# Kernel optimization log

Measured on AMD Instinct MI355X. Metric: run time of the kernel, lower is better.

## Reference

```python
import jax, jax.numpy as jnp
import numpy as np

N_EMBED = 1024
HEAD_SIZE = 64
SEQ_LEN = 4096
BATCH = 4


def setup_inputs() -> dict:
    key = jax.random.key(0)
    ks = jax.random.split(key, 7)
    scale = 1.0 / np.sqrt(N_EMBED)
    return {
        "x": jax.random.normal(ks[0], (BATCH, SEQ_LEN, N_EMBED), dtype=jnp.float32),
        "Wq": jax.random.normal(ks[1], (N_EMBED, HEAD_SIZE), dtype=jnp.float32) * scale,
        "bq": jax.random.normal(ks[2], (HEAD_SIZE,), dtype=jnp.float32) * 0.01,
        "Wk": jax.random.normal(ks[3], (N_EMBED, HEAD_SIZE), dtype=jnp.float32) * scale,
        "bk": jax.random.normal(ks[4], (HEAD_SIZE,), dtype=jnp.float32) * 0.01,
        "Wv": jax.random.normal(ks[5], (N_EMBED, HEAD_SIZE), dtype=jnp.float32) * scale,
        "bv": jax.random.normal(ks[6], (HEAD_SIZE,), dtype=jnp.float32) * 0.01,
    }


def reference(x, Wq, bq, Wk, bk, Wv, bv):
    # q, k, v: [B, S, H]
    q = x @ Wq + bq
    k = x @ Wk + bk
    v = x @ Wv + bv
    # raw scores [B, S, S]; original masks to -inf THEN divides by sqrt(head_size)
    # (-inf / sqrt = -inf, so equivalent to scaling finite entries only)
    scores = jnp.einsum("bqh,bkh->bqk", q, k)
    seq_len = x.shape[1]
    causal = jnp.tril(jnp.ones((seq_len, seq_len), dtype=bool))
    inv_scale = 1.0 / jnp.sqrt(jnp.asarray(HEAD_SIZE, dtype=scores.dtype))
    scores = jnp.where(causal, scores * inv_scale, -jnp.inf)
    weight = jax.nn.softmax(scores, axis=-1)
    # dropout is identity in eval / p=0
    out = jnp.einsum("bqk,bkh->bqh", weight, v)
    return out
```

## Files before the change

kernel.cpp:

```cpp
#include <hip/hip_runtime.h>
#include <hip/hip_bf16.h>

#define SS 4096
#define NROW 16384

typedef __attribute__((ext_vector_type(8))) short short8;
typedef __attribute__((ext_vector_type(4))) float f32x4;

#define AS1 __attribute__((address_space(1)))
#define AS3 __attribute__((address_space(3)))

static __device__ __forceinline__ void glds16(const void* g, void* l) {
    __builtin_amdgcn_global_load_lds((const AS1 unsigned*)g, (AS3 unsigned*)l, 16, 0, 0);
}
static __device__ __forceinline__ short f2bf(float f) {
    union { float f; unsigned u; } v; v.f = f;
    unsigned r = v.u + 0x7FFFu + ((v.u >> 16) & 1u);
    return (short)(r >> 16);
}
static __device__ __forceinline__ short f2bf_fast(float f) {
    union { float f; unsigned u; } v; v.f = f;
    return (short)((v.u + 0x8000u) >> 16);
}
static __device__ __forceinline__ unsigned pkbf(float lo, float hi) {
    union { float f; unsigned u; } x, y; x.f = lo; y.f = hi;
    return __builtin_amdgcn_perm(y.u + 0x8000u, x.u + 0x8000u, 0x07060302);
}
static __device__ __forceinline__ float bf2f(short s) {
    union { unsigned u; float f; } v;
    v.u = ((unsigned)(unsigned short)s) << 16;
    return v.f;
}

__global__ __launch_bounds__(256) void pack_w(const float* __restrict__ Wq,
                                              const float* __restrict__ Wk,
                                              const float* __restrict__ Wv,
                                              short* __restrict__ Wpack) {
    __shared__ float T[64 * 65];
    int bid = blockIdx.x;
    int nb = bid >> 4, kb = bid & 15;
    const float* W = (nb == 0) ? Wq : (nb == 1 ? Wk : Wv);
    int n0 = nb * 64, k0 = kb * 64;
    int tid = threadIdx.x;
    for (int ps = 0; ps < 16; ++ps) {
        int idx = tid + ps * 256;
        int kk = idx >> 6, nn = idx & 63;
        T[kk * 65 + nn] = W[(k0 + kk) * 64 + nn];
    }
    __syncthreads();
    for (int ps = 0; ps < 16; ++ps) {
        int idx = tid + ps * 256;
        int nn = idx >> 6, kk = idx & 63;
        Wpack[(n0 + nn) * 1024 + k0 + kk] = f2bf(T[kk * 65 + nn]);
    }
}

__global__ __launch_bounds__(256, 2) void proj_qkv(const float* __restrict__ x,
                                                   const short* __restrict__ Wpack,
                                                   const float* __restrict__ bq,
                                                   const float* __restrict__ bk,
                                                   const float* __restrict__ bv,
                                                   short* __restrict__ Qg,
                                                   short* __restrict__ Kg,
                                                   short* __restrict__ Vt) {
    __shared__ float Xs[2][32 * 64];
    __shared__ short Wsm[2][192 * 64];
    int tid = threadIdx.x, lane = tid & 63, wv = tid >> 6;
    int g = lane >> 4, c = lane & 15;
    int mh = wv & 1, nh = wv >> 1;
    int rowbase = blockIdx.x * 32;

    f32x4 acc[6];
    for (int i = 0; i < 6; ++i) acc[i] = (f32x4)(0.f);

    int xs0 = (wv * 2 + 0) * 64 + lane, xs1 = (wv * 2 + 1) * 64 + lane;
    int xr0 = xs0 >> 4, xp0 = (xs0 & 15) ^ (xr0 & 15);
    int xr1 = xs1 >> 4, xp1 = (xs1 & 15) ^ (xr1 & 15);

#define PROJ_ISSUE(nbs, k0)                                                              \
    do {                                                                                 \
        glds16(x + (rowbase + xr0) * 1024 + (k0) + xp0 * 4, &Xs[nbs][(wv * 2 + 0) * 256]); \
        glds16(x + (rowbase + xr1) * 1024 + (k0) + xp1 * 4, &Xs[nbs][(wv * 2 + 1) * 256]); \
        for (int j = 0; j < 6; ++j) {                                                    \
            int ws = (wv * 6 + j) * 64 + lane;                                           \
            int wr = ws >> 3, wp = (ws & 7) ^ (wr & 7);                                  \
            glds16(Wpack + wr * 1024 + (k0) + wp * 8, &Wsm[nbs][(wv * 6 + j) * 512]);    \
        }                                                                                \
    } while (0)

    PROJ_ISSUE(0, 0);

    for (int ko = 0; ko < 16; ++ko) {
        int bs = ko & 1;
        __syncthreads();
        if (ko < 15) PROJ_ISSUE(bs ^ 1, (ko + 1) * 64);
        for (int kc = 0; kc < 2; ++kc) {
            int h0 = kc * 8 + g * 2;
            float4 xa = *reinterpret_cast<const float4*>(&Xs[bs][(mh * 16 + c) * 64 + ((h0) ^ c) * 4]);
            float4 xb = *reinterpret_cast<const float4*>(&Xs[bs][(mh * 16 + c) * 64 + ((h0 + 1) ^ c) * 4]);
            short8 a;
            unsigned* aw = (unsigned*)&a;
            aw[0] = pkbf(xa.x, xa.y); aw[1] = pkbf(xa.z, xa.w);
            aw[2] = pkbf(xb.x, xb.y); aw[3] = pkbf(xb.z, xb.w);
            for (int nt = 0; nt < 6; ++nt) {
                int wrow = nh * 96 + nt * 16 + c;
                short8 b = *reinterpret_cast<const short8*>(&Wsm[bs][wrow * 64 + ((g + 4 * kc) ^ (c & 7)) * 8]);
                acc[nt] = __builtin_amdgcn_mfma_f32_16x16x32_bf16(a, b, acc[nt], 0, 0, 0);
            }
        }
    }
#undef PROJ_ISSUE

    const float SCQ = 0.125f * 1.4426950408889634f;
    for (int nt = 0; nt < 6; ++nt) {
        int col = nh * 96 + nt * 16 + c;
        for (int r = 0; r < 4; ++r) {
            int grow = rowbase + mh * 16 + g * 4 + r;
            float vv = acc[nt][r];
            if (col < 64) {
                Qg[grow * 64 + col] = f2bf((vv + bq[col]) * SCQ);
            } else if (col < 128) {
                Kg[grow * 64 + (col - 64)] = f2bf(vv + bk[col - 64]);
            } else {
                int f = col - 128;
                int batch = grow >> 12, s = grow & 4095;
                Vt[batch * 262144 + (s >> 6) * 4096 + f * 64 + (s & 63)] = f2bf(vv + bv[f]);
            }
        }
    }
}

__global__ __launch_bounds__(256, 3) void attn(const short* __restrict__ Qg,
                                               const short* __restrict__ Kg,
                                               const short* __restrict__ Vt,
                                               short* __restrict__ Opart,
                                               float* __restrict__ Ls) {
    __shared__ short Kbuf[2][64 * 64];
    __shared__ short Vbuf[2][64 * 64];
    __shared__ short Ps[4][16 * 68];
    int tid = threadIdx.x, lane = tid & 63, wv = tid >> 6;
    int g = lane >> 4, c = lane & 15;

    int bid = blockIdx.x;
    int batch = bid / 288;
    int j = bid - batch * 288;
    int gq = (int)((sqrtf((float)j + 1.0f) - 1.0f) * 0.5f);
    while (4 * (gq + 1) * (gq + 2) <= j) ++gq;
    while (4 * gq * (gq + 1) > j) --gq;
    int rem = j - 4 * gq * (gq + 1);
    int pidx = rem / (gq + 1);
    int ch = rem - pidx * (gq + 1);
    int p = gq * 8 + pidx;

    int ntall = p + 1;
    int t0 = ch * 8, t1 = min(t0 + 8, ntall);
    int qrow0 = batch * SS + p * 64;
    const short* Kb = Kg + batch * SS * 64;
    const short* Vb = Vt + batch * SS * 64;

    short8 aq0 = *reinterpret_cast<const short8*>(Qg + (qrow0 + wv * 16 + c) * 64 + g * 8);
    short8 aq1 = *reinterpret_cast<const short8*>(Qg + (qrow0 + wv * 16 + c) * 64 + 32 + g * 8);

    f32x4 acc_o[4];
    for (int f = 0; f < 4; ++f) acc_o[f] = (f32x4)(0.f);
    float rs[4] = {0.f, 0.f, 0.f, 0.f};

    int s0 = (wv * 2 + 0) * 64 + lane, s1 = (wv * 2 + 1) * 64 + lane;
    int r0 = s0 >> 3, q0 = ((s0 & 7) ^ (r0 & 7));
    int r1 = s1 >> 3, q1 = ((s1 & 7) ^ (r1 & 7));

#define ATTN_ISSUE(nbs, t)                                                           \
    do {                                                                             \
        const short* kt_ = Kb + (t) * 4096;                                          \
        const short* vt_ = Vb + (t) * 4096;                                          \
        glds16(kt_ + r0 * 64 + q0 * 8, &Kbuf[nbs][(wv * 2 + 0) * 512]);              \
        glds16(kt_ + r1 * 64 + q1 * 8, &Kbuf[nbs][(wv * 2 + 1) * 512]);              \
        glds16(vt_ + r0 * 64 + q0 * 8, &Vbuf[nbs][(wv * 2 + 0) * 512]);              \
        glds16(vt_ + r1 * 64 + q1 * 8, &Vbuf[nbs][(wv * 2 + 1) * 512]);              \
    } while (0)

    ATTN_ISSUE(0, t0);
    short* Psw = Ps[wv];

    for (int t = t0; t < t1; ++t) {
        int bs = (t - t0) & 1;
        __syncthreads();
        if (t + 1 < t1) ATTN_ISSUE(bs ^ 1, t + 1);

        f32x4 s[4];
        for (int nt = 0; nt < 4; ++nt) s[nt] = (f32x4)(0.f);
        for (int nt = 0; nt < 4; ++nt) {
            short8 b0 = *reinterpret_cast<const short8*>(&Kbuf[bs][(nt * 16 + c) * 64 + ((g) ^ (c & 7)) * 8]);
            s[nt] = __builtin_amdgcn_mfma_f32_16x16x32_bf16(aq0, b0, s[nt], 0, 0, 0);
            short8 b1 = *reinterpret_cast<const short8*>(&Kbuf[bs][(nt * 16 + c) * 64 + ((g + 4) ^ (c & 7)) * 8]);
            s[nt] = __builtin_amdgcn_mfma_f32_16x16x32_bf16(aq1, b1, s[nt], 0, 0, 0);
        }

        if (t == p) {
            for (int nt = 0; nt < 4; ++nt)
                for (int r = 0; r < 4; ++r) {
                    int key = nt * 16 + c;
                    int row = wv * 16 + g * 4 + r;
                    float pv = (key <= row) ? __builtin_amdgcn_exp2f(s[nt][r]) : 0.f;
                    rs[r] += pv;
                    Psw[(g * 4 + r) * 68 + nt * 16 + c] = f2bf_fast(pv);
                }
        } else {
            for (int nt = 0; nt < 4; ++nt)
                for (int r = 0; r < 4; ++r) {
                    float pv = __builtin_amdgcn_exp2f(s[nt][r]);
                    rs[r] += pv;
                    Psw[(g * 4 + r) * 68 + nt * 16 + c] = f2bf_fast(pv);
                }
        }

        for (int kc2 = 0; kc2 < 2; ++kc2) {
            short8 ap = *reinterpret_cast<const short8*>(&Psw[c * 68 + kc2 * 32 + g * 8]);
            for (int f = 0; f < 4; ++f) {
                short8 bv_ = *reinterpret_cast<const short8*>(&Vbuf[bs][(f * 16 + c) * 64 + ((g + 4 * kc2) ^ (c & 7)) * 8]);
                acc_o[f] = __builtin_amdgcn_mfma_f32_16x16x32_bf16(ap, bv_, acc_o[f], 0, 0, 0);
            }
        }
    }
#undef ATTN_ISSUE

    float l[4];
    for (int r = 0; r < 4; ++r) {
        float ss = rs[r];
        ss += __shfl_xor(ss, 1);
        ss += __shfl_xor(ss, 2);
        ss += __shfl_xor(ss, 4);
        ss += __shfl_xor(ss, 8);
        l[r] = ss;
    }

    int slot = ((batch * 64 + p) << 3) + ch;
    short* op = Opart + slot * 4096;
    for (int r = 0; r < 4; ++r) {
        float inv = 1.0f / l[r];
        int row = wv * 16 + g * 4 + r;
        for (int f = 0; f < 4; ++f)
            op[row * 64 + f * 16 + c] = f2bf(acc_o[f][r] * inv);
    }
    if (c == 0)
        for (int r = 0; r < 4; ++r)
            Ls[slot * 64 + wv * 16 + g * 4 + r] = l[r];
}

__global__ __launch_bounds__(256) void merge_k(const short* __restrict__ Opart,
                                               const float* __restrict__ Ls,
                                               float* __restrict__ out) {
    int bP = blockIdx.x;
    int P = bP & 63, batch = bP >> 6;
    int nch = (P + 8) >> 3;
    int tid = threadIdx.x;
    int row = tid & 63, fg = tid >> 6;
    int slot0 = bP << 3;

    float w[8];
    float wsum = 0.f;
    for (int i = 0; i < nch; ++i) { w[i] = Ls[(slot0 + i) * 64 + row]; wsum += w[i]; }
    float invw = 1.0f / wsum;

    float o[16];
    for (int jj = 0; jj < 16; ++jj) o[jj] = 0.f;
    for (int i = 0; i < nch; ++i) {
        const short* op = Opart + (slot0 + i) * 4096 + row * 64 + fg * 16;
        short8 v0 = *reinterpret_cast<const short8*>(op);
        short8 v1 = *reinterpret_cast<const short8*>(op + 8);
        for (int jj = 0; jj < 8; ++jj) {
            o[jj]     += w[i] * bf2f(v0[jj]);
            o[8 + jj] += w[i] * bf2f(v1[jj]);
        }
    }
    int orow = batch * SS + P * 64 + row;
    for (int jj = 0; jj < 16; jj += 4) {
        float4 v;
        v.x = o[jj] * invw; v.y = o[jj + 1] * invw; v.z = o[jj + 2] * invw; v.w = o[jj + 3] * invw;
        *reinterpret_cast<float4*>(out + orow * 64 + fg * 16 + jj) = v;
    }
}

extern "C" void kernel_launch(void* const* d_in, const int* in_sizes, int n_in,
                              void* d_out, int out_size, void* d_ws, size_t ws_size,
                              hipStream_t stream) {
    const float* x  = (const float*)d_in[0];
    const float* Wq = (const float*)d_in[1];
    const float* bq = (const float*)d_in[2];
    const float* Wk = (const float*)d_in[3];
    const float* bk = (const float*)d_in[4];
    const float* Wv = (const float*)d_in[5];
    const float* bv = (const float*)d_in[6];
    float* out = (float*)d_out;

    short* Wpack = (short*)d_ws;
    short* Qg    = Wpack + 196608;
    short* Kg    = Qg + NROW * 64;
    short* Vt    = Kg + NROW * 64;
    short* Opart = Vt + NROW * 64;
    float* Ls    = (float*)(Opart + 2048 * 4096);

    hipLaunchKernelGGL(pack_w,   dim3(48),   dim3(256), 0, stream, Wq, Wk, Wv, Wpack);
    hipLaunchKernelGGL(proj_qkv, dim3(512),  dim3(256), 0, stream, x, Wpack, bq, bk, bv, Qg, Kg, Vt);
    hipLaunchKernelGGL(attn,     dim3(1152), dim3(256), 0, stream, Qg, Kg, Vt, Opart, Ls);
    hipLaunchKernelGGL(merge_k,  dim3(256),  dim3(256), 0, stream, Opart, Ls, out);
}
```

Before: 163.1 us.

## Replace LDS staging with direct register loads in projection and attention

Both the projection and attention kernels drop the LDS double-buffered global_load_lds staging and __syncthreads. Operands are now loaded straight from global memory into MFMA register fragments, with a one-step software prefetch. The projection is retiled to 16 rows per block over 1024 blocks, and attention blocks are launched in reverse order so the long causal rows start first. This removes barrier and LDS traffic and raises occupancy, but each wave now loads K/V and W itself, so the same data is fetched repeatedly from global memory/L2 instead of once into shared memory.

```diff
diff --git a/kernel.cpp b/kernel.cpp
--- a/kernel.cpp
+++ b/kernel.cpp
@@ -7,12 +7,6 @@
 typedef __attribute__((ext_vector_type(8))) short short8;
 typedef __attribute__((ext_vector_type(4))) float f32x4;
 
-#define AS1 __attribute__((address_space(1)))
-#define AS3 __attribute__((address_space(3)))
-
-static __device__ __forceinline__ void glds16(const void* g, void* l) {
-    __builtin_amdgcn_global_load_lds((const AS1 unsigned*)g, (AS3 unsigned*)l, 16, 0, 0);
-}
 static __device__ __forceinline__ short f2bf(float f) {
     union { float f; unsigned u; } v; v.f = f;
     unsigned r = v.u + 0x7FFFu + ((v.u >> 16) & 1u);
@@ -55,7 +49,7 @@
     }
 }
 
-__global__ __launch_bounds__(256, 2) void proj_qkv(const float* __restrict__ x,
+__global__ __launch_bounds__(256, 4) void proj_qkv(const float* __restrict__ x,
                                                    const short* __restrict__ Wpack,
                                                    const float* __restrict__ bq,
                                                    const float* __restrict__ bk,
@@ -63,59 +57,51 @@
                                                    short* __restrict__ Qg,
                                                    short* __restrict__ Kg,
                                                    short* __restrict__ Vt) {
-    __shared__ float Xs[2][32 * 64];
-    __shared__ short Wsm[2][192 * 64];
     int tid = threadIdx.x, lane = tid & 63, wv = tid >> 6;
     int g = lane >> 4, c = lane & 15;
-    int mh = wv & 1, nh = wv >> 1;
-    int rowbase = blockIdx.x * 32;
-
-    f32x4 acc[6];
-    for (int i = 0; i < 6; ++i) acc[i] = (f32x4)(0.f);
-
-    int xs0 = (wv * 2 + 0) * 64 + lane, xs1 = (wv * 2 + 1) * 64 + lane;
-    int xr0 = xs0 >> 4, xp0 = (xs0 & 15) ^ (xr0 & 15);
-    int xr1 = xs1 >> 4, xp1 = (xs1 & 15) ^ (xr1 & 15);
-
-#define PROJ_ISSUE(nbs, k0)                                                              \
-    do {                                                                                 \
-        glds16(x + (rowbase + xr0) * 1024 + (k0) + xp0 * 4, &Xs[nbs][(wv * 2 + 0) * 256]); \
-        glds16(x + (rowbase + xr1) * 1024 + (k0) + xp1 * 4, &Xs[nbs][(wv * 2 + 1) * 256]); \
-        for (int j = 0; j < 6; ++j) {                                                    \
-            int ws = (wv * 6 + j) * 64 + lane;                                           \
-            int wr = ws >> 3, wp = (ws & 7) ^ (wr & 7);                                  \
-            glds16(Wpack + wr * 1024 + (k0) + wp * 8, &Wsm[nbs][(wv * 6 + j) * 512]);    \
-        }                                                                                \
-    } while (0)
-
-    PROJ_ISSUE(0, 0);
-
-    for (int ko = 0; ko < 16; ++ko) {
-        int bs = ko & 1;
-        __syncthreads();
-        if (ko < 15) PROJ_ISSUE(bs ^ 1, (ko + 1) * 64);
-        for (int kc = 0; kc < 2; ++kc) {
-            int h0 = kc * 8 + g * 2;
-            float4 xa = *reinterpret_cast<const float4*>(&Xs[bs][(mh * 16 + c) * 64 + ((h0) ^ c) * 4]);
-            float4 xb = *reinterpret_cast<const float4*>(&Xs[bs][(mh * 16 + c) * 64 + ((h0 + 1) ^ c) * 4]);
-            short8 a;
-            unsigned* aw = (unsigned*)&a;
-            aw[0] = pkbf(xa.x, xa.y); aw[1] = pkbf(xa.z, xa.w);
-            aw[2] = pkbf(xb.x, xb.y); aw[3] = pkbf(xb.z, xb.w);
-            for (int nt = 0; nt < 6; ++nt) {
-                int wrow = nh * 96 + nt * 16 + c;
-                short8 b = *reinterpret_cast<const short8*>(&Wsm[bs][wrow * 64 + ((g + 4 * kc) ^ (c & 7)) * 8]);
-                acc[nt] = __builtin_amdgcn_mfma_f32_16x16x32_bf16(a, b, acc[nt], 0, 0, 0);
-            }
-        }
-    }
-#undef PROJ_ISSUE
+    int rowbase = blockIdx.x * 16;
+    int col0 = wv * 48;
+
+    f32x4 acc[3];
+    for (int i = 0; i < 3; ++i) acc[i] = (f32x4)(0.f);
+
+    const float* xr = x + (rowbase + c) * 1024 + g * 8;
+    const short* wr = Wpack + (col0 + c) * 1024 + g * 8;
+
+    float4 xa = *reinterpret_cast<const float4*>(xr);
+    float4 xb = *reinterpret_cast<const float4*>(xr + 4);
+    short8 bcur[3];
+#pragma unroll
+    for (int nt = 0; nt < 3; ++nt)
+        bcur[nt] = *reinterpret_cast<const short8*>(wr + nt * 16384);
+
+    for (int ko = 0; ko < 32; ++ko) {
+        short8 a;
+        unsigned* aw = (unsigned*)&a;
+        aw[0] = pkbf(xa.x, xa.y); aw[1] = pkbf(xa.z, xa.w);
+        aw[2] = pkbf(xb.x, xb.y); aw[3] = pkbf(xb.z, xb.w);
+        short8 bnext[3];
+        if (ko < 31) {
+            int k1 = (ko + 1) * 32;
+            xa = *reinterpret_cast<const float4*>(xr + k1);
+            xb = *reinterpret_cast<const float4*>(xr + k1 + 4);
+#pragma unroll
+            for (int nt = 0; nt < 3; ++nt)
+                bnext[nt] = *reinterpret_cast<const short8*>(wr + nt * 16384 + k1);
+        }
+#pragma unroll
+        for (int nt = 0; nt < 3; ++nt)
+            acc[nt] = __builtin_amdgcn_mfma_f32_16x16x32_bf16(a, bcur[nt], acc[nt], 0, 0, 0);
+#pragma unroll
+        for (int nt = 0; nt < 3; ++nt) bcur[nt] = bnext[nt];
+    }
 
     const float SCQ = 0.125f * 1.4426950408889634f;
-    for (int nt = 0; nt < 6; ++nt) {
-        int col = nh * 96 + nt * 16 + c;
+#pragma unroll
+    for (int nt = 0; nt < 3; ++nt) {
+        int col = col0 + nt * 16 + c;
         for (int r = 0; r < 4; ++r) {
-            int grow = rowbase + mh * 16 + g * 4 + r;
+            int grow = rowbase + g * 4 + r;
             float vv = acc[nt][r];
             if (col < 64) {
                 Qg[grow * 64 + col] = f2bf((vv + bq[col]) * SCQ);
@@ -130,20 +116,18 @@
     }
 }
 
-__global__ __launch_bounds__(256, 3) void attn(const short* __restrict__ Qg,
+__global__ __launch_bounds__(256, 4) void attn(const short* __restrict__ Qg,
                                                const short* __restrict__ Kg,
                                                const short* __restrict__ Vt,
                                                short* __restrict__ Opart,
                                                float* __restrict__ Ls) {
-    __shared__ short Kbuf[2][64 * 64];
-    __shared__ short Vbuf[2][64 * 64];
     __shared__ short Ps[4][16 * 68];
     int tid = threadIdx.x, lane = tid & 63, wv = tid >> 6;
     int g = lane >> 4, c = lane & 15;
 
-    int bid = blockIdx.x;
-    int batch = bid / 288;
-    int j = bid - batch * 288;
+    int rb = 1151 - blockIdx.x;
+    int batch = rb / 288;
+    int j = rb - batch * 288;
     int gq = (int)((sqrtf((float)j + 1.0f) - 1.0f) * 0.5f);
     while (4 * (gq + 1) * (gq + 2) <= j) ++gq;
     while (4 * gq * (gq + 1) > j) --gq;
@@ -152,11 +136,10 @@
     int ch = rem - pidx * (gq + 1);
     int p = gq * 8 + pidx;
 
-    int ntall = p + 1;
-    int t0 = ch * 8, t1 = min(t0 + 8, ntall);
+    int t0 = ch * 8, t1 = min(t0 + 8, p + 1);
     int qrow0 = batch * SS + p * 64;
-    const short* Kb = Kg + batch * SS * 64;
-    const short* Vb = Vt + batch * SS * 64;
+    const short* KbL = Kg + batch * SS * 64 + c * 64 + g * 8;
+    const short* VbL = Vt + batch * SS * 64 + c * 64 + g * 8;
 
     short8 aq0 = *reinterpret_cast<const short8*>(Qg + (qrow0 + wv * 16 + c) * 64 + g * 8);
     short8 aq1 = *reinterpret_cast<const short8*>(Qg + (qrow0 + wv * 16 + c) * 64 + 32 + g * 8);
@@ -164,39 +147,33 @@
     f32x4 acc_o[4];
     for (int f = 0; f < 4; ++f) acc_o[f] = (f32x4)(0.f);
     float rs[4] = {0.f, 0.f, 0.f, 0.f};
-
-    int s0 = (wv * 2 + 0) * 64 + lane, s1 = (wv * 2 + 1) * 64 + lane;
-    int r0 = s0 >> 3, q0 = ((s0 & 7) ^ (r0 & 7));
-    int r1 = s1 >> 3, q1 = ((s1 & 7) ^ (r1 & 7));
-
-#define ATTN_ISSUE(nbs, t)                                                           \
-    do {                                                                             \
-        const short* kt_ = Kb + (t) * 4096;                                          \
-        const short* vt_ = Vb + (t) * 4096;                                          \
-        glds16(kt_ + r0 * 64 + q0 * 8, &Kbuf[nbs][(wv * 2 + 0) * 512]);              \
-        glds16(kt_ + r1 * 64 + q1 * 8, &Kbuf[nbs][(wv * 2 + 1) * 512]);              \
-        glds16(vt_ + r0 * 64 + q0 * 8, &Vbuf[nbs][(wv * 2 + 0) * 512]);              \
-        glds16(vt_ + r1 * 64 + q1 * 8, &Vbuf[nbs][(wv * 2 + 1) * 512]);              \
-    } while (0)
-
-    ATTN_ISSUE(0, t0);
     short* Psw = Ps[wv];
 
+    short8 kf[8];
+#pragma unroll
+    for (int i = 0; i < 8; ++i)
+        kf[i] = *reinterpret_cast<const short8*>(KbL + t0 * 4096 + (i & 3) * 1024 + (i >> 2) * 32);
+
     for (int t = t0; t < t1; ++t) {
-        int bs = (t - t0) & 1;
-        __syncthreads();
-        if (t + 1 < t1) ATTN_ISSUE(bs ^ 1, t + 1);
-
         f32x4 s[4];
-        for (int nt = 0; nt < 4; ++nt) s[nt] = (f32x4)(0.f);
+#pragma unroll
         for (int nt = 0; nt < 4; ++nt) {
-            short8 b0 = *reinterpret_cast<const short8*>(&Kbuf[bs][(nt * 16 + c) * 64 + ((g) ^ (c & 7)) * 8]);
-            s[nt] = __builtin_amdgcn_mfma_f32_16x16x32_bf16(aq0, b0, s[nt], 0, 0, 0);
-            short8 b1 = *reinterpret_cast<const short8*>(&Kbuf[bs][(nt * 16 + c) * 64 + ((g + 4) ^ (c & 7)) * 8]);
-            s[nt] = __builtin_amdgcn_mfma_f32_16x16x32_bf16(aq1, b1, s[nt], 0, 0, 0);
+            s[nt] = (f32x4)(0.f);
+            s[nt] = __builtin_amdgcn_mfma_f32_16x16x32_bf16(aq0, kf[nt], s[nt], 0, 0, 0);
+            s[nt] = __builtin_amdgcn_mfma_f32_16x16x32_bf16(aq1, kf[4 + nt], s[nt], 0, 0, 0);
+        }
+        short8 vf[8];
+#pragma unroll
+        for (int i = 0; i < 8; ++i)
+            vf[i] = *reinterpret_cast<const short8*>(VbL + t * 4096 + (i & 3) * 1024 + (i >> 2) * 32);
+        if (t + 1 < t1) {
+#pragma unroll
+            for (int i = 0; i < 8; ++i)
+                kf[i] = *reinterpret_cast<const short8*>(KbL + (t + 1) * 4096 + (i & 3) * 1024 + (i >> 2) * 32);
         }
 
         if (t == p) {
+#pragma unroll
             for (int nt = 0; nt < 4; ++nt)
                 for (int r = 0; r < 4; ++r) {
                     int key = nt * 16 + c;
@@ -206,6 +183,7 @@
                     Psw[(g * 4 + r) * 68 + nt * 16 + c] = f2bf_fast(pv);
                 }
         } else {
+#pragma unroll
             for (int nt = 0; nt < 4; ++nt)
                 for (int r = 0; r < 4; ++r) {
                     float pv = __builtin_amdgcn_exp2f(s[nt][r]);
@@ -214,17 +192,17 @@
                 }
         }
 
+#pragma unroll
         for (int kc2 = 0; kc2 < 2; ++kc2) {
             short8 ap = *reinterpret_cast<const short8*>(&Psw[c * 68 + kc2 * 32 + g * 8]);
-            for (int f = 0; f < 4; ++f) {
-                short8 bv_ = *reinterpret_cast<const short8*>(&Vbuf[bs][(f * 16 + c) * 64 + ((g + 4 * kc2) ^ (c & 7)) * 8]);
-                acc_o[f] = __builtin_amdgcn_mfma_f32_16x16x32_bf16(ap, bv_, acc_o[f], 0, 0, 0);
-            }
-        }
-    }
-#undef ATTN_ISSUE
+#pragma unroll
+            for (int ft = 0; ft < 4; ++ft)
+                acc_o[ft] = __builtin_amdgcn_mfma_f32_16x16x32_bf16(ap, vf[kc2 * 4 + ft], acc_o[ft], 0, 0, 0);
+        }
+    }
 
     float l[4];
+#pragma unroll
     for (int r = 0; r < 4; ++r) {
         float ss = rs[r];
         ss += __shfl_xor(ss, 1);
@@ -236,13 +214,15 @@
 
     int slot = ((batch * 64 + p) << 3) + ch;
     short* op = Opart + slot * 4096;
+#pragma unroll
     for (int r = 0; r < 4; ++r) {
         float inv = 1.0f / l[r];
         int row = wv * 16 + g * 4 + r;
-        for (int f = 0; f < 4; ++f)
-            op[row * 64 + f * 16 + c] = f2bf(acc_o[f][r] * inv);
+        for (int ft = 0; ft < 4; ++ft)
+            op[row * 64 + ft * 16 + c] = f2bf(acc_o[ft][r] * inv);
     }
     if (c == 0)
+#pragma unroll
         for (int r = 0; r < 4; ++r)
             Ls[slot * 64 + wv * 16 + g * 4 + r] = l[r];
 }
@@ -301,7 +281,7 @@
     float* Ls    = (float*)(Opart + 2048 * 4096);
 
     hipLaunchKernelGGL(pack_w,   dim3(48),   dim3(256), 0, stream, Wq, Wk, Wv, Wpack);
-    hipLaunchKernelGGL(proj_qkv, dim3(512),  dim3(256), 0, stream, x, Wpack, bq, bk, bv, Qg, Kg, Vt);
+    hipLaunchKernelGGL(proj_qkv, dim3(1024), dim3(256), 0, stream, x, Wpack, bq, bk, bv, Qg, Kg, Vt);
     hipLaunchKernelGGL(attn,     dim3(1152), dim3(256), 0, stream, Qg, Kg, Vt, Opart, Ls);
     hipLaunchKernelGGL(merge_k,  dim3(256),  dim3(256), 0, stream, Opart, Ls, out);
 }
```

After: 256.0 us. 1.57x slower.

## Keep P in registers via transposed QK^T and fp16 PV MFMA

Applied to the files above, without the earlier changes.

Computes S transposed (K as the A operand) so each lane holds probabilities in the layout the 16x16x16 f16 MFMA expects as its B operand. This removes the per-wave LDS round-trip for P. V is now stored as fp16 with an XOR swizzle by the projection kernel, and loaded straight into LDS without the extra swizzle. It also raises occupancy to 4 blocks per CU, launches blocks in reverse order so the heavier causal tiles start first, and writes the output with short4 vector stores. The costs are fp16 precision for P and V, and twice as many smaller MFMAs for the PV product.

```diff
diff --git a/kernel.cpp b/kernel.cpp
--- a/kernel.cpp
+++ b/kernel.cpp
@@ -6,6 +6,7 @@
 
 typedef __attribute__((ext_vector_type(8))) short short8;
 typedef __attribute__((ext_vector_type(4))) float f32x4;
+typedef _Float16 half4 __attribute__((ext_vector_type(4)));
 
 #define AS1 __attribute__((address_space(1)))
 #define AS3 __attribute__((address_space(3)))
@@ -17,10 +18,6 @@
     union { float f; unsigned u; } v; v.f = f;
     unsigned r = v.u + 0x7FFFu + ((v.u >> 16) & 1u);
     return (short)(r >> 16);
-}
-static __device__ __forceinline__ short f2bf_fast(float f) {
-    union { float f; unsigned u; } v; v.f = f;
-    return (short)((v.u + 0x8000u) >> 16);
 }
 static __device__ __forceinline__ unsigned pkbf(float lo, float hi) {
     union { float f; unsigned u; } x, y; x.f = lo; y.f = hi;
@@ -112,6 +109,7 @@
 #undef PROJ_ISSUE
 
     const float SCQ = 0.125f * 1.4426950408889634f;
+    _Float16* Vh = (_Float16*)Vt;
     for (int nt = 0; nt < 6; ++nt) {
         int col = nh * 96 + nt * 16 + c;
         for (int r = 0; r < 4; ++r) {
@@ -124,26 +122,27 @@
             } else {
                 int f = col - 128;
                 int batch = grow >> 12, s = grow & 4095;
-                Vt[batch * 262144 + (s >> 6) * 4096 + f * 64 + (s & 63)] = f2bf(vv + bv[f]);
+                int key = s & 63;
+                Vh[batch * 262144 + (s >> 6) * 4096 + f * 64 + (key ^ ((f & 15) * 4))] =
+                    (_Float16)(vv + bv[f]);
             }
         }
     }
 }
 
-__global__ __launch_bounds__(256, 3) void attn(const short* __restrict__ Qg,
+__global__ __launch_bounds__(256, 4) void attn(const short* __restrict__ Qg,
                                                const short* __restrict__ Kg,
                                                const short* __restrict__ Vt,
                                                short* __restrict__ Opart,
                                                float* __restrict__ Ls) {
     __shared__ short Kbuf[2][64 * 64];
     __shared__ short Vbuf[2][64 * 64];
-    __shared__ short Ps[4][16 * 68];
     int tid = threadIdx.x, lane = tid & 63, wv = tid >> 6;
     int g = lane >> 4, c = lane & 15;
 
-    int bid = blockIdx.x;
-    int batch = bid / 288;
-    int j = bid - batch * 288;
+    int rb = 1151 - blockIdx.x;
+    int batch = rb / 288;
+    int j = rb - batch * 288;
     int gq = (int)((sqrtf((float)j + 1.0f) - 1.0f) * 0.5f);
     while (4 * (gq + 1) * (gq + 2) <= j) ++gq;
     while (4 * gq * (gq + 1) > j) --gq;
@@ -152,8 +151,7 @@
     int ch = rem - pidx * (gq + 1);
     int p = gq * 8 + pidx;
 
-    int ntall = p + 1;
-    int t0 = ch * 8, t1 = min(t0 + 8, ntall);
+    int t0 = ch * 8, t1 = min(t0 + 8, p + 1);
     int qrow0 = batch * SS + p * 64;
     const short* Kb = Kg + batch * SS * 64;
     const short* Vb = Vt + batch * SS * 64;
@@ -163,24 +161,21 @@
 
     f32x4 acc_o[4];
     for (int f = 0; f < 4; ++f) acc_o[f] = (f32x4)(0.f);
-    float rs[4] = {0.f, 0.f, 0.f, 0.f};
-
-    int s0 = (wv * 2 + 0) * 64 + lane, s1 = (wv * 2 + 1) * 64 + lane;
-    int r0 = s0 >> 3, q0 = ((s0 & 7) ^ (r0 & 7));
-    int r1 = s1 >> 3, q1 = ((s1 & 7) ^ (r1 & 7));
-
-#define ATTN_ISSUE(nbs, t)                                                           \
-    do {                                                                             \
-        const short* kt_ = Kb + (t) * 4096;                                          \
-        const short* vt_ = Vb + (t) * 4096;                                          \
-        glds16(kt_ + r0 * 64 + q0 * 8, &Kbuf[nbs][(wv * 2 + 0) * 512]);              \
-        glds16(kt_ + r1 * 64 + q1 * 8, &Kbuf[nbs][(wv * 2 + 1) * 512]);              \
-        glds16(vt_ + r0 * 64 + q0 * 8, &Vbuf[nbs][(wv * 2 + 0) * 512]);              \
-        glds16(vt_ + r1 * 64 + q1 * 8, &Vbuf[nbs][(wv * 2 + 1) * 512]);              \
+    float rs = 0.f;
+
+    int s0 = wv * 128 + lane, s1 = s0 + 64;
+    int r0 = s0 >> 3, q0 = (s0 & 7) ^ (r0 & 7);
+    int r1 = s1 >> 3, q1 = (s1 & 7) ^ (r1 & 7);
+
+#define ATTN_ISSUE(nbs, t)                                                  \
+    do {                                                                    \
+        glds16(Kb + (t) * 4096 + r0 * 64 + q0 * 8, &Kbuf[nbs][s0 * 8]);     \
+        glds16(Kb + (t) * 4096 + r1 * 64 + q1 * 8, &Kbuf[nbs][s1 * 8]);     \
+        glds16(Vb + (t) * 4096 + s0 * 8, &Vbuf[nbs][s0 * 8]);               \
+        glds16(Vb + (t) * 4096 + s1 * 8, &Vbuf[nbs][s1 * 8]);               \
     } while (0)
 
     ATTN_ISSUE(0, t0);
-    short* Psw = Ps[wv];
 
     for (int t = t0; t < t1; ++t) {
         int bs = (t - t0) & 1;
@@ -188,63 +183,67 @@
         if (t + 1 < t1) ATTN_ISSUE(bs ^ 1, t + 1);
 
         f32x4 s[4];
-        for (int nt = 0; nt < 4; ++nt) s[nt] = (f32x4)(0.f);
+#pragma unroll
         for (int nt = 0; nt < 4; ++nt) {
-            short8 b0 = *reinterpret_cast<const short8*>(&Kbuf[bs][(nt * 16 + c) * 64 + ((g) ^ (c & 7)) * 8]);
-            s[nt] = __builtin_amdgcn_mfma_f32_16x16x32_bf16(aq0, b0, s[nt], 0, 0, 0);
-            short8 b1 = *reinterpret_cast<const short8*>(&Kbuf[bs][(nt * 16 + c) * 64 + ((g + 4) ^ (c & 7)) * 8]);
-            s[nt] = __builtin_amdgcn_mfma_f32_16x16x32_bf16(aq1, b1, s[nt], 0, 0, 0);
-        }
-
+            short8 k0 = *reinterpret_cast<const short8*>(&Kbuf[bs][(nt * 16 + c) * 64 + ((g) ^ (c & 7)) * 8]);
+            short8 k1 = *reinterpret_cast<const short8*>(&Kbuf[bs][(nt * 16 + c) * 64 + ((g + 4) ^ (c & 7)) * 8]);
+            s[nt] = (f32x4)(0.f);
+            s[nt] = __builtin_amdgcn_mfma_f32_16x16x32_bf16(k0, aq0, s[nt], 0, 0, 0);
+            s[nt] = __builtin_amdgcn_mfma_f32_16x16x32_bf16(k1, aq1, s[nt], 0, 0, 0);
+        }
+
+        half4 pb[4];
         if (t == p) {
+#pragma unroll
             for (int nt = 0; nt < 4; ++nt)
                 for (int r = 0; r < 4; ++r) {
-                    int key = nt * 16 + c;
-                    int row = wv * 16 + g * 4 + r;
+                    int key = nt * 16 + g * 4 + r;
+                    int row = wv * 16 + c;
                     float pv = (key <= row) ? __builtin_amdgcn_exp2f(s[nt][r]) : 0.f;
-                    rs[r] += pv;
-                    Psw[(g * 4 + r) * 68 + nt * 16 + c] = f2bf_fast(pv);
+                    rs += pv;
+                    pb[nt][r] = (_Float16)pv;
                 }
         } else {
+#pragma unroll
             for (int nt = 0; nt < 4; ++nt)
                 for (int r = 0; r < 4; ++r) {
                     float pv = __builtin_amdgcn_exp2f(s[nt][r]);
-                    rs[r] += pv;
-                    Psw[(g * 4 + r) * 68 + nt * 16 + c] = f2bf_fast(pv);
+                    rs += pv;
+                    pb[nt][r] = (_Float16)pv;
                 }
         }
 
-        for (int kc2 = 0; kc2 < 2; ++kc2) {
-            short8 ap = *reinterpret_cast<const short8*>(&Psw[c * 68 + kc2 * 32 + g * 8]);
-            for (int f = 0; f < 4; ++f) {
-                short8 bv_ = *reinterpret_cast<const short8*>(&Vbuf[bs][(f * 16 + c) * 64 + ((g + 4 * kc2) ^ (c & 7)) * 8]);
-                acc_o[f] = __builtin_amdgcn_mfma_f32_16x16x32_bf16(ap, bv_, acc_o[f], 0, 0, 0);
+#pragma unroll
+        for (int nt = 0; nt < 4; ++nt) {
+#pragma unroll
+            for (int ft = 0; ft < 4; ++ft) {
+                half4 va = *reinterpret_cast<const half4*>(
+                    &Vbuf[bs][(ft * 16 + c) * 64 + ((nt * 16 + g * 4) ^ (c * 4))]);
+                acc_o[ft] = __builtin_amdgcn_mfma_f32_16x16x16f16(va, pb[nt], acc_o[ft], 0, 0, 0);
             }
         }
     }
 #undef ATTN_ISSUE
 
-    float l[4];
-    for (int r = 0; r < 4; ++r) {
-        float ss = rs[r];
-        ss += __shfl_xor(ss, 1);
-        ss += __shfl_xor(ss, 2);
-        ss += __shfl_xor(ss, 4);
-        ss += __shfl_xor(ss, 8);
-        l[r] = ss;
-    }
+    float l = rs;
+    l += __shfl_xor(l, 16);
+    l += __shfl_xor(l, 32);
+    float inv = 1.0f / l;
 
     int slot = ((batch * 64 + p) << 3) + ch;
     short* op = Opart + slot * 4096;
-    for (int r = 0; r < 4; ++r) {
-        float inv = 1.0f / l[r];
-        int row = wv * 16 + g * 4 + r;
-        for (int f = 0; f < 4; ++f)
-            op[row * 64 + f * 16 + c] = f2bf(acc_o[f][r] * inv);
-    }
-    if (c == 0)
-        for (int r = 0; r < 4; ++r)
-            Ls[slot * 64 + wv * 16 + g * 4 + r] = l[r];
+    int row = wv * 16 + c;
+#pragma unroll
+    for (int ft = 0; ft < 4; ++ft) {
+        short4 ov;
+        ov.x = f2bf(acc_o[ft][0] * inv);
+        ov.y = f2bf(acc_o[ft][1] * inv);
+        ov.z = f2bf(acc_o[ft][2] * inv);
+        ov.w = f2bf(acc_o[ft][3] * inv);
+        *reinterpret_cast<short4*>(op + row * 64 + ft * 16 + g * 4) = ov;
+    }
+    if (g == 0)
+        Ls[slot * 64 + wv * 16 + c] = l;
 }
 
 __global__ __launch_bounds__(256) void merge_k(const short* __restrict__ Opart,
```

Measured after the change: 152.1 us. -6.7%, faster.
